# Kernel tuning notes

Measured on AMD Instinct MI355X. Metric: run time of the kernel, lower is better.

The kernel has to match this reference:

```python
import jax, jax.numpy as jnp
import numpy as np

TEMPERATURE = 0.5
EPS = 1e-8  # torch cosine_similarity norm clamp


def setup_inputs() -> dict:
    key = jax.random.key(0)
    k1, k2, k3 = jax.random.split(key, 3)
    N, D = 4096, 256
    z_i = jax.random.normal(k1, (N, D), dtype=jnp.float32)
    z_j = jax.random.normal(k2, (N, D), dtype=jnp.float32)
    weights = jax.random.uniform(k3, (N,), dtype=jnp.float32)
    return {"z_i": z_i, "z_j": z_j, "weights": weights}


def reference(z_i, z_j, weights):
    N = z_i.shape[0]
    z = jnp.concatenate([z_i, z_j], axis=0)  # [2N, D]
    # cosine similarity via normalized matmul (same math as broadcasted F.cosine_similarity)
    norm = jnp.maximum(jnp.linalg.norm(z, axis=1, keepdims=True), EPS)
    zn = z / norm
    sim = zn @ zn.T  # [2N, 2N]
    # positives: diagonals at offsets +N and -N
    sim_ij = jnp.diagonal(sim, offset=N)
    sim_ji = jnp.diagonal(sim, offset=-N)
    positives = jnp.concatenate([sim_ij, sim_ji], axis=0)  # [2N]
    mask = 1.0 - jnp.eye(2 * N, dtype=sim.dtype)
    denominator = jnp.sum(mask * jnp.exp(sim / TEMPERATURE), axis=1)  # [2N]
    numerator = jnp.exp(positives / TEMPERATURE)
    all_losses = -jnp.log(numerator / denominator)  # [2N]
    w2 = jnp.tile(weights, 2)  # weights.repeat(2)
    loss = jnp.sum(all_losses * w2) / jnp.sum(w2)
    return loss
```

## Files before the change

kernel.cpp:

```cpp
#include <hip/hip_runtime.h>
#include <hip/hip_bf16.h>
#include <hip/hip_fp8.h>

#define PN   4096
#define PN2  8192
#define PD   256
#define TILE 256
#define NBLK (PN2 / TILE)
#define NTRI (NBLK * (NBLK + 1) / 2)

typedef __attribute__((ext_vector_type(4))) float f32x4;
typedef const __attribute__((address_space(1))) void* gas_ptr;
typedef __attribute__((address_space(3))) void* las_ptr;

__device__ __forceinline__ void tri_decode(int idx, int& bi, int& bj) {
  bj = (int)((sqrtf(8.0f * (float)idx + 1.0f) - 1.0f) * 0.5f);
  while ((bj + 1) * (bj + 2) / 2 <= idx) ++bj;
  while (bj * (bj + 1) / 2 > idx) --bj;
  bi = idx - bj * (bj + 1) / 2;
}

__global__ __launch_bounds__(256) void normalize_kernel(
    const float* __restrict__ zi, const float* __restrict__ zj,
    unsigned char* __restrict__ zn8, float* __restrict__ pos,
    float* __restrict__ wlws, unsigned* __restrict__ ticket) {
  const int wave = threadIdx.x >> 6;
  const int lane = threadIdx.x & 63;
  const int r = blockIdx.x * 4 + wave;
  float4 a = *(const float4*)(zi + (size_t)r * PD + lane * 4);
  float4 b = *(const float4*)(zj + (size_t)r * PD + lane * 4);
  float si = a.x * a.x + a.y * a.y + a.z * a.z + a.w * a.w;
  float sj = b.x * b.x + b.y * b.y + b.z * b.z + b.w * b.w;
  float d  = a.x * b.x + a.y * b.y + a.z * b.z + a.w * b.w;
  #pragma unroll
  for (int off = 32; off >= 1; off >>= 1) {
    si += __shfl_xor(si, off, 64);
    sj += __shfl_xor(sj, off, 64);
    d  += __shfl_xor(d,  off, 64);
  }
  float ni = fmaxf(sqrtf(si), 1e-8f);
  float nj = fmaxf(sqrtf(sj), 1e-8f);
  if (lane == 0) {
    float p = d / (ni * nj);
    pos[r] = p;
    pos[r + PN] = p;
  }
  float ia = 1.0f / ni, ib = 1.0f / nj;
  union { unsigned u; unsigned char c[4]; } pa, pb;
  pa.c[0] = __hip_cvt_float_to_fp8(a.x * ia, __HIP_SATFINITE, __HIP_E4M3);
  pa.c[1] = __hip_cvt_float_to_fp8(a.y * ia, __HIP_SATFINITE, __HIP_E4M3);
  pa.c[2] = __hip_cvt_float_to_fp8(a.z * ia, __HIP_SATFINITE, __HIP_E4M3);
  pa.c[3] = __hip_cvt_float_to_fp8(a.w * ia, __HIP_SATFINITE, __HIP_E4M3);
  pb.c[0] = __hip_cvt_float_to_fp8(b.x * ib, __HIP_SATFINITE, __HIP_E4M3);
  pb.c[1] = __hip_cvt_float_to_fp8(b.y * ib, __HIP_SATFINITE, __HIP_E4M3);
  pb.c[2] = __hip_cvt_float_to_fp8(b.z * ib, __HIP_SATFINITE, __HIP_E4M3);
  pb.c[3] = __hip_cvt_float_to_fp8(b.w * ib, __HIP_SATFINITE, __HIP_E4M3);
  *(unsigned*)(zn8 + (size_t)r * PD + lane * 4) = pa.u;
  *(unsigned*)(zn8 + (size_t)(r + PN) * PD + lane * 4) = pb.u;
  if (blockIdx.x == 0 && threadIdx.x == 0) {
    wlws[0] = 0.0f; wlws[1] = 0.0f; *ticket = 0u;
  }
}

__global__ __launch_bounds__(512, 2) void simsum_kernel(
    const unsigned char* __restrict__ zn8, float* __restrict__ rowpart) {
  __shared__ char As[TILE * PD];
  __shared__ char Bs[TILE * PD];
  __shared__ float rowacc[TILE];
  __shared__ float colacc[TILE];

  const int tid = threadIdx.x;
  if (tid < TILE) { rowacc[tid] = 0.0f; colacc[tid] = 0.0f; }

  const int idx = (int)((blockIdx.x & 7) * (NTRI / 8) + (blockIdx.x >> 3));
  int bi, bj;
  tri_decode(idx, bi, bj);
  const bool diagBlk = (bi == bj);

  const int wave = tid >> 6;
  const int lane = tid & 63;
  const int quad = lane >> 4;
  const int c16  = lane & 15;
  const int rowBase = bi * TILE;
  const int colBase = bj * TILE;
  const int waveRow = (wave >> 2) * 128;
  const int waveCol = (wave & 3) * 64;

  #pragma unroll
  for (int p = 0; p < 8; ++p) {
    int issue = wave * 8 + p;
    int rr = issue * 4 + quad;
    int gs = c16 ^ (rr & 15);
    const unsigned char* ga = zn8 + (size_t)(rowBase + rr) * PD + gs * 16;
    __builtin_amdgcn_global_load_lds((gas_ptr)ga, (las_ptr)(As + issue * 1024), 16, 0, 0);
    if (!diagBlk) {
      const unsigned char* gb = zn8 + (size_t)(colBase + rr) * PD + gs * 16;
      __builtin_amdgcn_global_load_lds((gas_ptr)gb, (las_ptr)(Bs + issue * 1024), 16, 0, 0);
    }
  }
  __syncthreads();

  const char* BsEff = diagBlk ? As : Bs;

  f32x4 acc[8][4];
  #pragma unroll
  for (int i = 0; i < 8; ++i)
    #pragma unroll
    for (int j = 0; j < 4; ++j)
      acc[i][j] = (f32x4){0.f, 0.f, 0.f, 0.f};

  #pragma unroll
  for (int ki = 0; ki < 8; ++ki) {
    const int G  = ki * 2 + (quad >> 1);
    const int h8 = (quad & 1) * 8;
    long b[4];
    #pragma unroll
    for (int ni = 0; ni < 4; ++ni) {
      int r = waveCol + ni * 16 + c16;
      b[ni] = *(const long*)(BsEff + r * 256 + (((G ^ (r & 15)) << 4) + h8));
    }
    #pragma unroll
    for (int mi = 0; mi < 8; ++mi) {
      int r = waveRow + mi * 16 + c16;
      long a = *(const long*)(As + r * 256 + (((G ^ (r & 15)) << 4) + h8));
      #pragma unroll
      for (int ni = 0; ni < 4; ++ni)
        acc[mi][ni] = __builtin_amdgcn_mfma_f32_16x16x32_fp8_fp8(a, b[ni], acc[mi][ni], 0, 0, 0);
    }
  }

  float colsum[4] = {0.f, 0.f, 0.f, 0.f};
  #pragma unroll
  for (int mi = 0; mi < 8; ++mi) {
    int lrow = waveRow + mi * 16 + quad * 4;
    float rs[4] = {0.f, 0.f, 0.f, 0.f};
    #pragma unroll
    for (int ni = 0; ni < 4; ++ni) {
      int gcol = colBase + waveCol + ni * 16 + c16;
      #pragma unroll
      for (int t = 0; t < 4; ++t) {
        int grow = rowBase + lrow + t;
        float e = __expf(2.0f * acc[mi][ni][t]);
        if (diagBlk && gcol == grow) e = 0.0f;
        rs[t] += e;
        colsum[ni] += e;
      }
    }
    #pragma unroll
    for (int t = 0; t < 4; ++t) {
      #pragma unroll
      for (int off = 1; off <= 8; off <<= 1) rs[t] += __shfl_xor(rs[t], off, 64);
    }
    if (c16 == 0) {
      #pragma unroll
      for (int t = 0; t < 4; ++t) atomicAdd(&rowacc[lrow + t], rs[t]);
    }
  }
  if (!diagBlk) {
    #pragma unroll
    for (int ni = 0; ni < 4; ++ni) {
      float cs = colsum[ni];
      cs += __shfl_xor(cs, 16, 64);
      cs += __shfl_xor(cs, 32, 64);
      if (quad == 0) atomicAdd(&colacc[waveCol + ni * 16 + c16], cs);
    }
  }

  __syncthreads();
  if (tid < TILE) {
    rowpart[(size_t)bj * PN2 + rowBase + tid] = rowacc[tid];
    if (!diagBlk)
      rowpart[(size_t)bi * PN2 + colBase + tid] = colacc[tid];
  }
}

__global__ __launch_bounds__(256) void finalize_kernel(
    const float* __restrict__ rowpart, const float* __restrict__ pos,
    const float* __restrict__ w, float* __restrict__ wlws,
    unsigned* __restrict__ ticket, float* __restrict__ out) {
  const int tid = threadIdx.x;
  const int r = blockIdx.x * 256 + tid;
  float s = 0.0f;
  #pragma unroll
  for (int x = 0; x < NBLK; ++x) s += rowpart[(size_t)x * PN2 + r];
  float li = logf(s) - 2.0f * pos[r];
  float wi = w[r & (PN - 1)];
  float wl = wi * li, ws = wi;
  #pragma unroll
  for (int off = 32; off >= 1; off >>= 1) {
    wl += __shfl_xor(wl, off, 64);
    ws += __shfl_xor(ws, off, 64);
  }
  __shared__ float pl[4], pw[4];
  const int lane = tid & 63, wv = tid >> 6;
  if (lane == 0) { pl[wv] = wl; pw[wv] = ws; }
  __syncthreads();
  if (tid == 0) {
    atomicAdd(&wlws[0], pl[0] + pl[1] + pl[2] + pl[3]);
    atomicAdd(&wlws[1], pw[0] + pw[1] + pw[2] + pw[3]);
    __threadfence();
    if (atomicAdd(ticket, 1u) == 31) {
      float a = atomicAdd(&wlws[0], 0.0f);
      float b = atomicAdd(&wlws[1], 0.0f);
      out[0] = a / b;
    }
  }
}

extern "C" void kernel_launch(void* const* d_in, const int* in_sizes, int n_in,
                              void* d_out, int out_size, void* d_ws, size_t ws_size,
                              hipStream_t stream) {
  const float* zi = (const float*)d_in[0];
  const float* zj = (const float*)d_in[1];
  const float* w  = (const float*)d_in[2];
  float* out = (float*)d_out;

  unsigned char* zn8 = (unsigned char*)d_ws;
  float* rowpart = (float*)((char*)d_ws + (size_t)PN2 * PD);
  float* pos     = rowpart + (size_t)NBLK * PN2;
  float* wlws    = pos + PN2;
  unsigned* ticket = (unsigned*)(wlws + 2);

  normalize_kernel<<<PN / 4, 256, 0, stream>>>(zi, zj, zn8, pos, wlws, ticket);
  simsum_kernel<<<NTRI, 512, 0, stream>>>(zn8, rowpart);
  finalize_kernel<<<32, 256, 0, stream>>>(rowpart, pos, w, wlws, ticket, out);
}
```

Baseline: 103.1 us.

## Make similarity kernel persistent with 256 blocks and reuse staged column tile

Replaces the one-block-per-triangle-tile launch of 528 blocks with a persistent grid of 256 blocks, each walking a contiguous run of about two triangular tiles. When consecutive tiles share the same column block, the B tile already in shared memory is reused instead of reloaded. Launch bounds drop to one block per CU. The loop is serialized within a block with no overlap between loading the next tile and computing the current one, so the gain in reuse may be offset by lower occupancy and exposed load latency.

```diff
diff --git a/kernel.cpp b/kernel.cpp
--- a/kernel.cpp
+++ b/kernel.cpp
@@ -8,6 +8,7 @@
 #define TILE 256
 #define NBLK (PN2 / TILE)
 #define NTRI (NBLK * (NBLK + 1) / 2)
+#define SGRID 256
 
 typedef __attribute__((ext_vector_type(4))) float f32x4;
 typedef const __attribute__((address_space(1))) void* gas_ptr;
@@ -62,115 +63,127 @@
   }
 }
 
-__global__ __launch_bounds__(512, 2) void simsum_kernel(
+__global__ __launch_bounds__(512, 1) void simsum_kernel(
     const unsigned char* __restrict__ zn8, float* __restrict__ rowpart) {
   __shared__ char As[TILE * PD];
   __shared__ char Bs[TILE * PD];
   __shared__ float rowacc[TILE];
   __shared__ float colacc[TILE];
 
-  const int tid = threadIdx.x;
-  if (tid < TILE) { rowacc[tid] = 0.0f; colacc[tid] = 0.0f; }
-
-  const int idx = (int)((blockIdx.x & 7) * (NTRI / 8) + (blockIdx.x >> 3));
-  int bi, bj;
-  tri_decode(idx, bi, bj);
-  const bool diagBlk = (bi == bj);
-
+  const int tid  = threadIdx.x;
   const int wave = tid >> 6;
   const int lane = tid & 63;
   const int quad = lane >> 4;
   const int c16  = lane & 15;
-  const int rowBase = bi * TILE;
-  const int colBase = bj * TILE;
   const int waveRow = (wave >> 2) * 128;
   const int waveCol = (wave & 3) * 64;
 
-  #pragma unroll
-  for (int p = 0; p < 8; ++p) {
-    int issue = wave * 8 + p;
-    int rr = issue * 4 + quad;
-    int gs = c16 ^ (rr & 15);
-    const unsigned char* ga = zn8 + (size_t)(rowBase + rr) * PD + gs * 16;
-    __builtin_amdgcn_global_load_lds((gas_ptr)ga, (las_ptr)(As + issue * 1024), 16, 0, 0);
+  const int vb = ((int)blockIdx.x & 7) * 32 + ((int)blockIdx.x >> 3);
+  int idx = (vb * 33) >> 4;
+  const int idxEnd = ((vb + 1) * 33) >> 4;
+  int bi, bj;
+  tri_decode(idx, bi, bj);
+  int curBj = -1;
+
+  for (; idx < idxEnd; ++idx) {
+    const bool diagBlk = (bi == bj);
+    const bool stageB  = (!diagBlk) && (bj != curBj);
+    const int rowBase = bi * TILE;
+    const int colBase = bj * TILE;
+
+    if (tid < TILE) { rowacc[tid] = 0.0f; colacc[tid] = 0.0f; }
+
+    #pragma unroll
+    for (int p = 0; p < 8; ++p) {
+      int issue = wave * 8 + p;
+      int rr = issue * 4 + quad;
+      int gs = c16 ^ (rr & 15);
+      const unsigned char* ga = zn8 + (size_t)(rowBase + rr) * PD + gs * 16;
+      __builtin_amdgcn_global_load_lds((gas_ptr)ga, (las_ptr)(As + issue * 1024), 16, 0, 0);
+      if (stageB) {
+        const unsigned char* gb = zn8 + (size_t)(colBase + rr) * PD + gs * 16;
+        __builtin_amdgcn_global_load_lds((gas_ptr)gb, (las_ptr)(Bs + issue * 1024), 16, 0, 0);
+      }
+    }
+    if (stageB) curBj = bj;
+    __syncthreads();
+
+    const char* BsEff = diagBlk ? As : Bs;
+
+    f32x4 acc[8][4];
+    #pragma unroll
+    for (int i = 0; i < 8; ++i)
+      #pragma unroll
+      for (int j = 0; j < 4; ++j)
+        acc[i][j] = (f32x4){0.f, 0.f, 0.f, 0.f};
+
+    #pragma unroll
+    for (int ki = 0; ki < 8; ++ki) {
+      const int G  = ki * 2 + (quad >> 1);
+      const int h8 = (quad & 1) * 8;
+      long b[4];
+      #pragma unroll
+      for (int ni = 0; ni < 4; ++ni) {
+        int r = waveCol + ni * 16 + c16;
+        b[ni] = *(const long*)(BsEff + r * 256 + (((G ^ (r & 15)) << 4) + h8));
+      }
+      #pragma unroll
+      for (int mi = 0; mi < 8; ++mi) {
+        int r = waveRow + mi * 16 + c16;
+        long a = *(const long*)(As + r * 256 + (((G ^ (r & 15)) << 4) + h8));
+        #pragma unroll
+        for (int ni = 0; ni < 4; ++ni)
+          acc[mi][ni] = __builtin_amdgcn_mfma_f32_16x16x32_fp8_fp8(a, b[ni], acc[mi][ni], 0, 0, 0);
+      }
+    }
+
+    float colsum[4] = {0.f, 0.f, 0.f, 0.f};
+    #pragma unroll
+    for (int mi = 0; mi < 8; ++mi) {
+      int lrow = waveRow + mi * 16 + quad * 4;
+      float rs[4] = {0.f, 0.f, 0.f, 0.f};
+      #pragma unroll
+      for (int ni = 0; ni < 4; ++ni) {
+        int gcol = colBase + waveCol + ni * 16 + c16;
+        #pragma unroll
+        for (int tt = 0; tt < 4; ++tt) {
+          int grow = rowBase + lrow + tt;
+          float e = __expf(2.0f * acc[mi][ni][tt]);
+          if (diagBlk && gcol == grow) e = 0.0f;
+          rs[tt] += e;
+          colsum[ni] += e;
+        }
+      }
+      #pragma unroll
+      for (int tt = 0; tt < 4; ++tt) {
+        #pragma unroll
+        for (int off = 1; off <= 8; off <<= 1) rs[tt] += __shfl_xor(rs[tt], off, 64);
+      }
+      if (c16 == 0) {
+        #pragma unroll
+        for (int tt = 0; tt < 4; ++tt) atomicAdd(&rowacc[lrow + tt], rs[tt]);
+      }
+    }
     if (!diagBlk) {
-      const unsigned char* gb = zn8 + (size_t)(colBase + rr) * PD + gs * 16;
-      __builtin_amdgcn_global_load_lds((gas_ptr)gb, (las_ptr)(Bs + issue * 1024), 16, 0, 0);
-    }
-  }
-  __syncthreads();
-
-  const char* BsEff = diagBlk ? As : Bs;
-
-  f32x4 acc[8][4];
-  #pragma unroll
-  for (int i = 0; i < 8; ++i)
-    #pragma unroll
-    for (int j = 0; j < 4; ++j)
-      acc[i][j] = (f32x4){0.f, 0.f, 0.f, 0.f};
-
-  #pragma unroll
-  for (int ki = 0; ki < 8; ++ki) {
-    const int G  = ki * 2 + (quad >> 1);
-    const int h8 = (quad & 1) * 8;
-    long b[4];
-    #pragma unroll
-    for (int ni = 0; ni < 4; ++ni) {
-      int r = waveCol + ni * 16 + c16;
-      b[ni] = *(const long*)(BsEff + r * 256 + (((G ^ (r & 15)) << 4) + h8));
-    }
-    #pragma unroll
-    for (int mi = 0; mi < 8; ++mi) {
-      int r = waveRow + mi * 16 + c16;
-      long a = *(const long*)(As + r * 256 + (((G ^ (r & 15)) << 4) + h8));
-      #pragma unroll
-      for (int ni = 0; ni < 4; ++ni)
-        acc[mi][ni] = __builtin_amdgcn_mfma_f32_16x16x32_fp8_fp8(a, b[ni], acc[mi][ni], 0, 0, 0);
-    }
-  }
-
-  float colsum[4] = {0.f, 0.f, 0.f, 0.f};
-  #pragma unroll
-  for (int mi = 0; mi < 8; ++mi) {
-    int lrow = waveRow + mi * 16 + quad * 4;
-    float rs[4] = {0.f, 0.f, 0.f, 0.f};
-    #pragma unroll
-    for (int ni = 0; ni < 4; ++ni) {
-      int gcol = colBase + waveCol + ni * 16 + c16;
-      #pragma unroll
-      for (int t = 0; t < 4; ++t) {
-        int grow = rowBase + lrow + t;
-        float e = __expf(2.0f * acc[mi][ni][t]);
-        if (diagBlk && gcol == grow) e = 0.0f;
-        rs[t] += e;
-        colsum[ni] += e;
-      }
-    }
-    #pragma unroll
-    for (int t = 0; t < 4; ++t) {
-      #pragma unroll
-      for (int off = 1; off <= 8; off <<= 1) rs[t] += __shfl_xor(rs[t], off, 64);
-    }
-    if (c16 == 0) {
-      #pragma unroll
-      for (int t = 0; t < 4; ++t) atomicAdd(&rowacc[lrow + t], rs[t]);
-    }
-  }
-  if (!diagBlk) {
-    #pragma unroll
-    for (int ni = 0; ni < 4; ++ni) {
-      float cs = colsum[ni];
-      cs += __shfl_xor(cs, 16, 64);
-      cs += __shfl_xor(cs, 32, 64);
-      if (quad == 0) atomicAdd(&colacc[waveCol + ni * 16 + c16], cs);
-    }
-  }
-
-  __syncthreads();
-  if (tid < TILE) {
-    rowpart[(size_t)bj * PN2 + rowBase + tid] = rowacc[tid];
-    if (!diagBlk)
-      rowpart[(size_t)bi * PN2 + colBase + tid] = colacc[tid];
+      #pragma unroll
+      for (int ni = 0; ni < 4; ++ni) {
+        float cs = colsum[ni];
+        cs += __shfl_xor(cs, 16, 64);
+        cs += __shfl_xor(cs, 32, 64);
+        if (quad == 0) atomicAdd(&colacc[waveCol + ni * 16 + c16], cs);
+      }
+    }
+
+    __syncthreads();
+    if (tid < TILE) {
+      rowpart[(size_t)bj * PN2 + rowBase + tid] = rowacc[tid];
+      if (!diagBlk)
+        rowpart[(size_t)bi * PN2 + colBase + tid] = colacc[tid];
+    }
+    __syncthreads();
+
+    ++bi;
+    if (bi > bj) { ++bj; bi = 0; }
   }
 }
 
@@ -222,6 +235,6 @@
   unsigned* ticket = (unsigned*)(wlws + 2);
 
   normalize_kernel<<<PN / 4, 256, 0, stream>>>(zi, zj, zn8, pos, wlws, ticket);
-  simsum_kernel<<<NTRI, 512, 0, stream>>>(zn8, rowpart);
+  simsum_kernel<<<SGRID, 512, 0, stream>>>(zn8, rowpart);
   finalize_kernel<<<32, 256, 0, stream>>>(rowpart, pos, w, wlws, ticket, out);
 }
```

Measured after the change: 103.7 us. Within noise of the previous version (+0.6%).
